# Optimization experiments

Measured on AMD Instinct MI355X. Metric: run time of the kernel, lower is better.

Reference implementation:

```python
import jax, jax.numpy as jnp
import numpy as np

B, N, K = 2, 50000, 16
CIN, COUT, M = 64, 32, 4


def setup_inputs() -> dict:
    key = jax.random.key(0)
    ks = jax.random.split(key, 7)
    x = jax.random.normal(ks[0], (B, N, CIN), dtype=jnp.float32)
    adj = jax.random.randint(ks[1], (B, N, K), 0, N + 1)  # 0 == empty slot
    weight = jax.random.normal(ks[2], (M, COUT, CIN), dtype=jnp.float32) * 0.1
    bias = jax.random.normal(ks[3], (COUT,), dtype=jnp.float32) * 0.1
    u = jax.random.normal(ks[4], (M, CIN), dtype=jnp.float32) * 0.1
    v = jax.random.normal(ks[5], (M, CIN), dtype=jnp.float32) * 0.1
    c = jax.random.normal(ks[6], (M,), dtype=jnp.float32) * 0.1
    return {"x": x, "adj": adj, "weight": weight, "bias": bias,
            "u": u, "v": v, "c": c}


def _gather_padded(feat, adj):
    # feat: (B, N, ...); adj: (B, N, K) indices into zero-padded node axis
    # (index 0 selects the zero row, matching torch get_patches semantics)
    pad = jnp.zeros((feat.shape[0], 1) + feat.shape[2:], feat.dtype)
    feat_p = jnp.concatenate([pad, feat], axis=1)        # (B, N+1, ...)
    return jax.vmap(lambda f, a: f[a])(feat_p, adj)      # (B, N, K, ...)


def reference(x, adj, weight, bias, u, v, c):
    # degree normalization: 1/#nonzero-neighbors, 0 for isolated points
    deg = jnp.sum(adj != 0, axis=-1).astype(x.dtype)     # (B, N)
    inv_deg = jnp.where(deg != 0, 1.0 / deg, 0.0)        # (B, N)

    # mixture-kernel transform of every node, then neighbor gather
    wx = jnp.einsum('bnc,moc->bnmo', x, weight)          # (B, N, M, COUT)
    gathered = _gather_padded(wx, adj)                   # (B, N, K, M, COUT)

    # softmax-gated assignment q[b,n,k,m] = softmax_m(v.x_nbr + u.x_ctr + c)
    ux = jnp.einsum('mc,bnc->bnm', u, x)                 # (B, N, M)
    vx = jnp.einsum('mc,bnc->bnm', v, x)                 # (B, N, M)
    vg = _gather_padded(vx, adj)                         # (B, N, K, M)
    q = jax.nn.softmax(vg + ux[:, :, None, :] + c, axis=-1)

    # weighted sum over neighbors K and mixture components M
    out = jnp.einsum('bnkm,bnkmo->bno', q, gathered)     # (B, N, COUT)
    return out * inv_deg[..., None] + bias
```

## Files before the change

### kernel.cpp

```cpp
#include <hip/hip_runtime.h>

namespace {
constexpr int BB = 2;
constexpr int NN = 50000;
constexpr int KK = 16;
constexpr int CI = 64;
constexpr int CO = 32;
constexpr int MM = 4;
constexpr int BN = BB * NN;
constexpr int GROUPS = NN / 4;
constexpr int GRID = 768;
constexpr int WAVES = (GRID / 2) * 4;
}

typedef __attribute__((ext_vector_type(8))) short short8v;
typedef __attribute__((ext_vector_type(4))) float float4v;
typedef __attribute__((ext_vector_type(2))) float f32x2;

union F4P {
  float4 f4;
  f32x2 p[2];
};

__device__ __forceinline__ unsigned short bf16r(float f) {
  unsigned int u = __float_as_uint(f);
  u += 0x7FFFu + ((u >> 16) & 1u);
  return (unsigned short)(u >> 16);
}

__global__ __launch_bounds__(256) void k_prep2(
    const float* __restrict__ x, const float* __restrict__ u,
    const float* __restrict__ v, float* __restrict__ ux,
    float* __restrict__ vx, unsigned short* __restrict__ xh) {
  const int tid = threadIdx.x;
  const int lane = tid & 63;
  const int wv = tid >> 6;
  const int col = lane & 15;
  const int krow = lane >> 4;

  short8v bfrag2[2];
#pragma unroll
  for (int ks = 0; ks < 2; ++ks)
#pragma unroll
    for (int e = 0; e < 8; ++e) {
      int c = ks * 32 + krow * 8 + e;
      float val = (col < 4) ? u[col * CI + c]
                            : ((col < 8) ? v[(col - 4) * CI + c] : 0.f);
      bfrag2[ks][e] = (short)bf16r(val);
    }

  const float4v zero = {0.f, 0.f, 0.f, 0.f};
  const int nw = gridDim.x * 4;
  for (int t = blockIdx.x * 4 + wv; t < BN / 16; t += nw) {
    const int n0 = t * 16;
    const float* xp = x + (size_t)(n0 + col) * CI + krow * 8;
    short8v afrag[2];
    uint4 hpack[2];
#pragma unroll
    for (int ks = 0; ks < 2; ++ks) {
      float4 lo = *(const float4*)(xp + ks * 32);
      float4 hi = *(const float4*)(xp + ks * 32 + 4);
      unsigned short h0 = bf16r(lo.x), h1 = bf16r(lo.y);
      unsigned short h2 = bf16r(lo.z), h3 = bf16r(lo.w);
      unsigned short h4 = bf16r(hi.x), h5 = bf16r(hi.y);
      unsigned short h6 = bf16r(hi.z), h7 = bf16r(hi.w);
      afrag[ks][0] = (short)h0;
      afrag[ks][1] = (short)h1;
      afrag[ks][2] = (short)h2;
      afrag[ks][3] = (short)h3;
      afrag[ks][4] = (short)h4;
      afrag[ks][5] = (short)h5;
      afrag[ks][6] = (short)h6;
      afrag[ks][7] = (short)h7;
      hpack[ks] = make_uint4((unsigned)h0 | ((unsigned)h1 << 16),
                             (unsigned)h2 | ((unsigned)h3 << 16),
                             (unsigned)h4 | ((unsigned)h5 << 16),
                             (unsigned)h6 | ((unsigned)h7 << 16));
    }
    unsigned short* xo = xh + (size_t)(n0 + col) * CI + krow * 8;
    *(uint4*)(xo) = hpack[0];
    *(uint4*)(xo + 32) = hpack[1];

    float4v acc2 = zero;
    acc2 = __builtin_amdgcn_mfma_f32_16x16x32_bf16(afrag[0], bfrag2[0], acc2,
                                                   0, 0, 0);
    acc2 = __builtin_amdgcn_mfma_f32_16x16x32_bf16(afrag[1], bfrag2[1], acc2,
                                                   0, 0, 0);
#pragma unroll
    for (int ri = 0; ri < 4; ++ri) {
      int node = n0 + krow * 4 + ri;
      if (col < 4)
        ux[(size_t)node * MM + col] = acc2[ri];
      else if (col < 8)
        vx[(size_t)node * MM + (col - 4)] = acc2[ri];
    }
  }
}

__global__ __launch_bounds__(256, 3) void k_gather(
    const unsigned short* __restrict__ xh, const int* __restrict__ adj,
    const float* __restrict__ weight, const float* __restrict__ bias,
    const float* __restrict__ cvec, const float* __restrict__ ux,
    const float* __restrict__ vx, float* __restrict__ out) {
  __shared__ unsigned short w_lds[2 * 8 * 64 * 8];
  __shared__ unsigned short t_lds[4][8 * 256];
  __shared__ float q_lds[4][4][64];

  const int tid = threadIdx.x;
  const int lane = tid & 63;
  const int wv = tid >> 6;

  for (int i = tid; i < 2 * 8 * 64; i += 256) {
    int tl = i >> 9;
    int ks = (i >> 6) & 7;
    int l = i & 63;
    int o = tl * 16 + (l & 15);
    unsigned pk[4];
#pragma unroll
    for (int ee = 0; ee < 4; ++ee) {
      int k0 = ks * 32 + (l >> 4) * 8 + 2 * ee;
      unsigned lo = bf16r(weight[((k0 & 3) * CO + o) * CI + (k0 >> 2)]);
      unsigned hi =
          bf16r(weight[(((k0 + 1) & 3) * CO + o) * CI + ((k0 + 1) >> 2)]);
      pk[ee] = lo | (hi << 16);
    }
    *(uint4*)&w_lds[i * 8] = make_uint4(pk[0], pk[1], pk[2], pk[3]);
  }
  __syncthreads();

  const int m4 = lane & 3;
  const int k4 = lane >> 2;
  const float cm = cvec[m4];
  const float b0 = bias[lane & 15];
  const float b1 = bias[16 + (lane & 15)];

  const int xcd = blockIdx.x & 7;
  const int b = xcd >> 2;
  const int wb = ((blockIdx.x >> 3) << 2) | (xcd & 3);
  const int w = wb * 4 + wv;
  const size_t bbase = (size_t)b * NN;
  const unsigned short* xhb = xh + bbase * CI;
  const float* vxb = vx + bbase * MM;
  unsigned short* twv = t_lds[wv];

#define LOADS(n, GV)                                                       \
  _Pragma("unroll") for (int k = 0; k < KK; ++k) {                         \
    int r = __builtin_amdgcn_readlane(av_c, (n)*16 + k);                   \
    const unsigned short* rp = xhb + (size_t)(max(r, 1) - 1) * CI;         \
    GV[k] = rp[lane];                                                      \
  }

#define ACC_NODE(n, GV)                                                    \
  {                                                                        \
    const float4* qp = (const float4*)&q_lds[wv][n][0];                    \
    f32x2 t01 = {0.f, 0.f}, t23 = {0.f, 0.f};                              \
    _Pragma("unroll") for (int k = 0; k < KK; ++k) {                       \
      float xv = __uint_as_float(GV[k] << 16);                             \
      F4P qv;                                                              \
      qv.f4 = qp[k];                                                       \
      t01 += qv.p[0] * xv;                                                 \
      t23 += qv.p[1] * xv;                                                 \
    }                                                                      \
    unsigned lo, hi;                                                       \
    asm("v_cvt_pk_bf16_f32 %0, %1, %2"                                     \
        : "=v"(lo)                                                         \
        : "v"(t01[0]), "v"(t01[1]));                                       \
    asm("v_cvt_pk_bf16_f32 %0, %1, %2"                                     \
        : "=v"(hi)                                                         \
        : "v"(t23[0]), "v"(t23[1]));                                       \
    int row = jrows * 4 + (n);                                             \
    unsigned boff = (unsigned)row * 512u +                                 \
                    (((unsigned)lane * 8u) ^ ((unsigned)(row & 7) << 4));  \
    *(uint2*)((char*)twv + boff) = make_uint2(lo, hi);                     \
  }

#define FLUSH(JC)                                                          \
  {                                                                        \
    float4v ac0 = {0.f, 0.f, 0.f, 0.f};                                    \
    float4v ac1 = {0.f, 0.f, 0.f, 0.f};                                    \
    const int arow = lane & 7;                                             \
    const unsigned axor = (unsigned)(arow & 7) << 4;                       \
    _Pragma("unroll") for (int ks = 0; ks < 8; ++ks) {                     \
      unsigned aoff =                                                      \
          (unsigned)arow * 512u +                                          \
          ((((unsigned)(lane >> 4)) * 16u + (unsigned)ks * 64u) ^ axor);   \
      short8v A = *(const short8v*)((const char*)twv + aoff);              \
      short8v Bl = *(const short8v*)&w_lds[(0 * 8 + ks) * 512 + lane * 8]; \
      short8v Bh = *(const short8v*)&w_lds[(1 * 8 + ks) * 512 + lane * 8]; \
      ac0 = __builtin_amdgcn_mfma_f32_16x16x32_bf16(A, Bl, ac0, 0, 0, 0);  \
      ac1 = __builtin_amdgcn_mfma_f32_16x16x32_bf16(A, Bh, ac1, 0, 0, 0);  \
    }                                                                      \
    int jj = lane >> 4;                                                    \
    int gg = gbase + jj * WAVES;                                           \
    if (jj < (JC) && gg < GROUPS) {                                        \
      float* op = out + (bbase + (size_t)gg * 4) * CO + (lane & 15);       \
      op[0] = ac0[0] + b0;                                                 \
      op[16] = ac1[0] + b1;                                                \
      op[32] = ac0[1] + b0;                                                \
      op[48] = ac1[1] + b1;                                                \
      op[64] = ac0[2] + b0;                                                \
      op[80] = ac1[2] + b1;                                                \
      op[96] = ac0[3] + b0;                                                \
      op[112] = ac1[3] + b1;                                               \
    }                                                                      \
  }

  int g = w;
  int av = 0;
  if (g < GROUPS) av = adj[(bbase + (size_t)g * 4) * KK + lane];
  int jrows = 0;
  int gbase = g;

  while (g < GROUPS) {
    const int av_c = av;
    const size_t bn0 = bbase + (size_t)g * 4;

    int as0 = __shfl(av_c, k4);
    int as1 = __shfl(av_c, 16 + k4);
    int as2 = __shfl(av_c, 32 + k4);
    int as3 = __shfl(av_c, 48 + k4);
    float vg0 = vxb[(size_t)(max(as0, 1) - 1) * MM + m4];
    float vg1 = vxb[(size_t)(max(as1, 1) - 1) * MM + m4];
    float vg2 = vxb[(size_t)(max(as2, 1) - 1) * MM + m4];
    float vg3 = vxb[(size_t)(max(as3, 1) - 1) * MM + m4];
    float ux0 = ux[bn0 * MM + m4];
    float ux1 = ux[(bn0 + 1) * MM + m4];
    float ux2 = ux[(bn0 + 2) * MM + m4];
    float ux3 = ux[(bn0 + 3) * MM + m4];
    const unsigned long long msk = __ballot(av_c != 0);

    unsigned gv0[KK], gv1[KK], gv2[KK], gv3[KK];
    LOADS(0, gv0)
    LOADS(1, gv1)
    LOADS(2, gv2)
    LOADS(3, gv3)
    __builtin_amdgcn_sched_barrier(0);

    const int gn = g + WAVES;
    if (gn < GROUPS) av = adj[(bbase + (size_t)gn * 4) * KK + lane];

    {
      int d0 = __popc((unsigned)(msk & 0xFFFFull));
      int d1 = __popc((unsigned)((msk >> 16) & 0xFFFFull));
      int d2 = __popc((unsigned)((msk >> 32) & 0xFFFFull));
      int d3 = __popc((unsigned)((msk >> 48) & 0xFFFFull));
      float i0 = d0 ? __builtin_amdgcn_rcpf((float)d0) : 0.f;
      float i1 = d1 ? __builtin_amdgcn_rcpf((float)d1) : 0.f;
      float i2 = d2 ? __builtin_amdgcn_rcpf((float)d2) : 0.f;
      float i3 = d3 ? __builtin_amdgcn_rcpf((float)d3) : 0.f;
      float e0 = __expf(vg0 + ux0 + cm);
      float e1 = __expf(vg1 + ux1 + cm);
      float e2 = __expf(vg2 + ux2 + cm);
      float e3 = __expf(vg3 + ux3 + cm);
      float s0 = e0 + __shfl_xor(e0, 1);
      float s1 = e1 + __shfl_xor(e1, 1);
      float s2 = e2 + __shfl_xor(e2, 1);
      float s3 = e3 + __shfl_xor(e3, 1);
      s0 += __shfl_xor(s0, 2);
      s1 += __shfl_xor(s1, 2);
      s2 += __shfl_xor(s2, 2);
      s3 += __shfl_xor(s3, 2);
      q_lds[wv][0][lane] =
          (as0 != 0) ? e0 * __builtin_amdgcn_rcpf(s0) * i0 : 0.f;
      q_lds[wv][1][lane] =
          (as1 != 0) ? e1 * __builtin_amdgcn_rcpf(s1) * i1 : 0.f;
      q_lds[wv][2][lane] =
          (as2 != 0) ? e2 * __builtin_amdgcn_rcpf(s2) * i2 : 0.f;
      q_lds[wv][3][lane] =
          (as3 != 0) ? e3 * __builtin_amdgcn_rcpf(s3) * i3 : 0.f;
    }

    ACC_NODE(0, gv0)
    ACC_NODE(1, gv1)
    ACC_NODE(2, gv2)
    ACC_NODE(3, gv3)

    ++jrows;
    g = gn;
    if (jrows == 2) {
      FLUSH(2)
      jrows = 0;
      gbase = g;
    }
  }
  if (jrows > 0) FLUSH(jrows)
}

__global__ __launch_bounds__(256) void k_uxvx(
    const float* __restrict__ x, const float* __restrict__ u,
    const float* __restrict__ v, float* __restrict__ ux,
    float* __restrict__ vx) {
  int idx = blockIdx.x * 256 + threadIdx.x;
  if (idx >= BN) return;
  const float4* xr = (const float4*)(x + (size_t)idx * CI);
  float su[MM] = {0.f, 0.f, 0.f, 0.f};
  float sv[MM] = {0.f, 0.f, 0.f, 0.f};
#pragma unroll
  for (int t = 0; t < CI / 4; ++t) {
    float4 xv = xr[t];
#pragma unroll
    for (int m = 0; m < MM; ++m) {
      float4 uv = *(const float4*)(u + m * CI + t * 4);
      float4 vv = *(const float4*)(v + m * CI + t * 4);
      su[m] += uv.x * xv.x + uv.y * xv.y + uv.z * xv.z + uv.w * xv.w;
      sv[m] += vv.x * xv.x + vv.y * xv.y + vv.z * xv.z + vv.w * xv.w;
    }
  }
  ((float4*)ux)[idx] = make_float4(su[0], su[1], su[2], su[3]);
  ((float4*)vx)[idx] = make_float4(sv[0], sv[1], sv[2], sv[3]);
}

__global__ __launch_bounds__(256) void k_main_old(
    const float* __restrict__ x, const int* __restrict__ adj,
    const float* __restrict__ weight, const float* __restrict__ bias,
    const float* __restrict__ cvec, const float* __restrict__ ux,
    const float* __restrict__ vx, float* __restrict__ out) {
  __shared__ float w_lds2[MM][CO][CI + 4];
  __shared__ float q_lds2[4][64];
  __shared__ float t_lds2[4][MM][CI];
  const int tid = threadIdx.x;
  const int lane = tid & 63;
  const int wv = tid >> 6;
#pragma unroll
  for (int i = 0; i < (MM * CO * CI) / 256; ++i) {
    int g = i * 256 + tid;
    w_lds2[g >> 11][(g >> 6) & (CO - 1)][g & (CI - 1)] = weight[g];
  }
  __syncthreads();
  const int k4 = lane >> 2;
  const int m4 = lane & 3;
  const int o = lane & 31;
  const int hh = lane >> 5;
  const float cm = cvec[m4];
  const float bo = bias[o];
  for (int g = blockIdx.x; g < BN / 4; g += gridDim.x) {
    const int bn = g * 4 + wv;
    const int b = (bn >= NN) ? 1 : 0;
    const int* adjp = adj + (size_t)bn * KK;
    const float* xb = x + (size_t)b * NN * CI;
    int4 A[4];
#pragma unroll
    for (int i = 0; i < 4; ++i) A[i] = ((const int4*)adjp)[i];
    int deg = 0;
#pragma unroll
    for (int i = 0; i < 4; ++i)
      deg += (A[i].x != 0) + (A[i].y != 0) + (A[i].z != 0) + (A[i].w != 0);
    const float inv_deg = (deg > 0) ? 1.0f / (float)deg : 0.0f;
    int a = adjp[k4];
    float vg = 0.f;
    if (a != 0) vg = vx[((size_t)b * NN + (a - 1)) * MM + m4];
    float logit = vg + ux[(size_t)bn * MM + m4] + cm;
    float mx = fmaxf(logit, __shfl_xor(logit, 1));
    mx = fmaxf(mx, __shfl_xor(mx, 2));
    float e = __expf(logit - mx);
    float s = e + __shfl_xor(e, 1);
    s += __shfl_xor(s, 2);
    q_lds2[wv][lane] = (a != 0) ? (e / s) : 0.f;
    int rows[KK];
    {
      int tmp[KK] = {A[0].x, A[0].y, A[0].z, A[0].w, A[1].x, A[1].y,
                     A[1].z, A[1].w, A[2].x, A[2].y, A[2].z, A[2].w,
                     A[3].x, A[3].y, A[3].z, A[3].w};
#pragma unroll
      for (int k = 0; k < KK; ++k) rows[k] = max(tmp[k], 1) - 1;
    }
    float xg[KK];
#pragma unroll
    for (int k = 0; k < KK; ++k) xg[k] = xb[(size_t)rows[k] * CI + lane];
    float t0 = 0.f, t1 = 0.f, t2 = 0.f, t3 = 0.f;
#pragma unroll
    for (int k = 0; k < KK; ++k) {
      float4 qv = *(const float4*)&q_lds2[wv][k * 4];
      t0 += qv.x * xg[k];
      t1 += qv.y * xg[k];
      t2 += qv.z * xg[k];
      t3 += qv.w * xg[k];
    }
    t_lds2[wv][0][lane] = t0;
    t_lds2[wv][1][lane] = t1;
    t_lds2[wv][2][lane] = t2;
    t_lds2[wv][3][lane] = t3;
    float a0 = 0.f, a1 = 0.f, a2 = 0.f, a3 = 0.f;
#pragma unroll
    for (int mm = 0; mm < 2; ++mm) {
      const float* wrow = &w_lds2[2 * hh + mm][o][0];
      const float* trow = &t_lds2[wv][2 * hh + mm][0];
#pragma unroll
      for (int t4 = 0; t4 < CI / 4; ++t4) {
        float4 wvv = *(const float4*)(wrow + 4 * t4);
        float4 tv = *(const float4*)(trow + 4 * t4);
        a0 += wvv.x * tv.x;
        a1 += wvv.y * tv.y;
        a2 += wvv.z * tv.z;
        a3 += wvv.w * tv.w;
      }
    }
    float acc = (a0 + a1) + (a2 + a3);
    acc += __shfl_xor(acc, 32);
    if (lane < 32) out[(size_t)bn * CO + o] = acc * inv_deg + bo;
  }
}

extern "C" void kernel_launch(void* const* d_in, const int* in_sizes, int n_in,
                              void* d_out, int out_size, void* d_ws,
                              size_t ws_size, hipStream_t stream) {
  const float* x = (const float*)d_in[0];
  const int* adj = (const int*)d_in[1];
  const float* weight = (const float*)d_in[2];
  const float* bias = (const float*)d_in[3];
  const float* u = (const float*)d_in[4];
  const float* v = (const float*)d_in[5];
  const float* cvec = (const float*)d_in[6];
  float* out = (float*)d_out;

  float* ux = (float*)d_ws;
  float* vx = ux + (size_t)BN * MM;
  const size_t base = (size_t)BN * MM * 2 * sizeof(float);
  const size_t xh_bytes = (size_t)BN * CI * sizeof(unsigned short);

  if (ws_size >= base + xh_bytes) {
    unsigned short* xhb = (unsigned short*)((char*)d_ws + base);
    k_prep2<<<1563, 256, 0, stream>>>(x, u, v, ux, vx, xhb);
    k_gather<<<GRID, 256, 0, stream>>>(xhb, adj, weight, bias, cvec, ux, vx,
                                       out);
  } else {
    k_uxvx<<<(BN + 255) / 256, 256, 0, stream>>>(x, u, v, ux, vx);
    k_main_old<<<1024, 256, 0, stream>>>(x, adj, weight, bias, cvec, ux, vx,
                                         out);
  }
}
```

Before: 62.53 us.

## Fuse prep and gather kernels into one cooperative kernel with grid sync

Merges the bf16 conversion / ux-vx projection kernel and the neighbour gather kernel into a single cooperative launch separated by a grid-wide barrier. Each block's prep work covers the same batch half it later gathers, and the weight LDS staging overlaps the prep phase. This removes one kernel launch and its inter-kernel gap. In exchange it adds a grid sync and depends on cooperative launch succeeding, with the old two-kernel path kept as a fallback.

```diff
diff --git a/kernel.cpp b/kernel.cpp
--- a/kernel.cpp
+++ b/kernel.cpp
@@ -1,4 +1,7 @@
 #include <hip/hip_runtime.h>
+#include <hip/hip_cooperative_groups.h>
+
+namespace cg = cooperative_groups;
 
 namespace {
 constexpr int BB = 2;
@@ -9,6 +12,7 @@
 constexpr int MM = 4;
 constexpr int BN = BB * NN;
 constexpr int GROUPS = NN / 4;
+constexpr int TILES = NN / 16;
 constexpr int GRID = 768;
 constexpr int WAVES = (GRID / 2) * 4;
 }
@@ -27,121 +31,6 @@
   u += 0x7FFFu + ((u >> 16) & 1u);
   return (unsigned short)(u >> 16);
 }
-
-__global__ __launch_bounds__(256) void k_prep2(
-    const float* __restrict__ x, const float* __restrict__ u,
-    const float* __restrict__ v, float* __restrict__ ux,
-    float* __restrict__ vx, unsigned short* __restrict__ xh) {
-  const int tid = threadIdx.x;
-  const int lane = tid & 63;
-  const int wv = tid >> 6;
-  const int col = lane & 15;
-  const int krow = lane >> 4;
-
-  short8v bfrag2[2];
-#pragma unroll
-  for (int ks = 0; ks < 2; ++ks)
-#pragma unroll
-    for (int e = 0; e < 8; ++e) {
-      int c = ks * 32 + krow * 8 + e;
-      float val = (col < 4) ? u[col * CI + c]
-                            : ((col < 8) ? v[(col - 4) * CI + c] : 0.f);
-      bfrag2[ks][e] = (short)bf16r(val);
-    }
-
-  const float4v zero = {0.f, 0.f, 0.f, 0.f};
-  const int nw = gridDim.x * 4;
-  for (int t = blockIdx.x * 4 + wv; t < BN / 16; t += nw) {
-    const int n0 = t * 16;
-    const float* xp = x + (size_t)(n0 + col) * CI + krow * 8;
-    short8v afrag[2];
-    uint4 hpack[2];
-#pragma unroll
-    for (int ks = 0; ks < 2; ++ks) {
-      float4 lo = *(const float4*)(xp + ks * 32);
-      float4 hi = *(const float4*)(xp + ks * 32 + 4);
-      unsigned short h0 = bf16r(lo.x), h1 = bf16r(lo.y);
-      unsigned short h2 = bf16r(lo.z), h3 = bf16r(lo.w);
-      unsigned short h4 = bf16r(hi.x), h5 = bf16r(hi.y);
-      unsigned short h6 = bf16r(hi.z), h7 = bf16r(hi.w);
-      afrag[ks][0] = (short)h0;
-      afrag[ks][1] = (short)h1;
-      afrag[ks][2] = (short)h2;
-      afrag[ks][3] = (short)h3;
-      afrag[ks][4] = (short)h4;
-      afrag[ks][5] = (short)h5;
-      afrag[ks][6] = (short)h6;
-      afrag[ks][7] = (short)h7;
-      hpack[ks] = make_uint4((unsigned)h0 | ((unsigned)h1 << 16),
-                             (unsigned)h2 | ((unsigned)h3 << 16),
-                             (unsigned)h4 | ((unsigned)h5 << 16),
-                             (unsigned)h6 | ((unsigned)h7 << 16));
-    }
-    unsigned short* xo = xh + (size_t)(n0 + col) * CI + krow * 8;
-    *(uint4*)(xo) = hpack[0];
-    *(uint4*)(xo + 32) = hpack[1];
-
-    float4v acc2 = zero;
-    acc2 = __builtin_amdgcn_mfma_f32_16x16x32_bf16(afrag[0], bfrag2[0], acc2,
-                                                   0, 0, 0);
-    acc2 = __builtin_amdgcn_mfma_f32_16x16x32_bf16(afrag[1], bfrag2[1], acc2,
-                                                   0, 0, 0);
-#pragma unroll
-    for (int ri = 0; ri < 4; ++ri) {
-      int node = n0 + krow * 4 + ri;
-      if (col < 4)
-        ux[(size_t)node * MM + col] = acc2[ri];
-      else if (col < 8)
-        vx[(size_t)node * MM + (col - 4)] = acc2[ri];
-    }
-  }
-}
-
-__global__ __launch_bounds__(256, 3) void k_gather(
-    const unsigned short* __restrict__ xh, const int* __restrict__ adj,
-    const float* __restrict__ weight, const float* __restrict__ bias,
-    const float* __restrict__ cvec, const float* __restrict__ ux,
-    const float* __restrict__ vx, float* __restrict__ out) {
-  __shared__ unsigned short w_lds[2 * 8 * 64 * 8];
-  __shared__ unsigned short t_lds[4][8 * 256];
-  __shared__ float q_lds[4][4][64];
-
-  const int tid = threadIdx.x;
-  const int lane = tid & 63;
-  const int wv = tid >> 6;
-
-  for (int i = tid; i < 2 * 8 * 64; i += 256) {
-    int tl = i >> 9;
-    int ks = (i >> 6) & 7;
-    int l = i & 63;
-    int o = tl * 16 + (l & 15);
-    unsigned pk[4];
-#pragma unroll
-    for (int ee = 0; ee < 4; ++ee) {
-      int k0 = ks * 32 + (l >> 4) * 8 + 2 * ee;
-      unsigned lo = bf16r(weight[((k0 & 3) * CO + o) * CI + (k0 >> 2)]);
-      unsigned hi =
-          bf16r(weight[(((k0 + 1) & 3) * CO + o) * CI + ((k0 + 1) >> 2)]);
-      pk[ee] = lo | (hi << 16);
-    }
-    *(uint4*)&w_lds[i * 8] = make_uint4(pk[0], pk[1], pk[2], pk[3]);
-  }
-  __syncthreads();
-
-  const int m4 = lane & 3;
-  const int k4 = lane >> 2;
-  const float cm = cvec[m4];
-  const float b0 = bias[lane & 15];
-  const float b1 = bias[16 + (lane & 15)];
-
-  const int xcd = blockIdx.x & 7;
-  const int b = xcd >> 2;
-  const int wb = ((blockIdx.x >> 3) << 2) | (xcd & 3);
-  const int w = wb * 4 + wv;
-  const size_t bbase = (size_t)b * NN;
-  const unsigned short* xhb = xh + bbase * CI;
-  const float* vxb = vx + bbase * MM;
-  unsigned short* twv = t_lds[wv];
 
 #define LOADS(n, GV)                                                       \
   _Pragma("unroll") for (int k = 0; k < KK; ++k) {                         \
@@ -205,85 +94,295 @@
     }                                                                      \
   }
 
-  int g = w;
-  int av = 0;
-  if (g < GROUPS) av = adj[(bbase + (size_t)g * 4) * KK + lane];
-  int jrows = 0;
-  int gbase = g;
-
-  while (g < GROUPS) {
-    const int av_c = av;
-    const size_t bn0 = bbase + (size_t)g * 4;
-
-    int as0 = __shfl(av_c, k4);
-    int as1 = __shfl(av_c, 16 + k4);
-    int as2 = __shfl(av_c, 32 + k4);
-    int as3 = __shfl(av_c, 48 + k4);
-    float vg0 = vxb[(size_t)(max(as0, 1) - 1) * MM + m4];
-    float vg1 = vxb[(size_t)(max(as1, 1) - 1) * MM + m4];
-    float vg2 = vxb[(size_t)(max(as2, 1) - 1) * MM + m4];
-    float vg3 = vxb[(size_t)(max(as3, 1) - 1) * MM + m4];
-    float ux0 = ux[bn0 * MM + m4];
-    float ux1 = ux[(bn0 + 1) * MM + m4];
-    float ux2 = ux[(bn0 + 2) * MM + m4];
-    float ux3 = ux[(bn0 + 3) * MM + m4];
-    const unsigned long long msk = __ballot(av_c != 0);
-
-    unsigned gv0[KK], gv1[KK], gv2[KK], gv3[KK];
-    LOADS(0, gv0)
-    LOADS(1, gv1)
-    LOADS(2, gv2)
-    LOADS(3, gv3)
-    __builtin_amdgcn_sched_barrier(0);
-
-    const int gn = g + WAVES;
-    if (gn < GROUPS) av = adj[(bbase + (size_t)gn * 4) * KK + lane];
-
-    {
-      int d0 = __popc((unsigned)(msk & 0xFFFFull));
-      int d1 = __popc((unsigned)((msk >> 16) & 0xFFFFull));
-      int d2 = __popc((unsigned)((msk >> 32) & 0xFFFFull));
-      int d3 = __popc((unsigned)((msk >> 48) & 0xFFFFull));
-      float i0 = d0 ? __builtin_amdgcn_rcpf((float)d0) : 0.f;
-      float i1 = d1 ? __builtin_amdgcn_rcpf((float)d1) : 0.f;
-      float i2 = d2 ? __builtin_amdgcn_rcpf((float)d2) : 0.f;
-      float i3 = d3 ? __builtin_amdgcn_rcpf((float)d3) : 0.f;
-      float e0 = __expf(vg0 + ux0 + cm);
-      float e1 = __expf(vg1 + ux1 + cm);
-      float e2 = __expf(vg2 + ux2 + cm);
-      float e3 = __expf(vg3 + ux3 + cm);
-      float s0 = e0 + __shfl_xor(e0, 1);
-      float s1 = e1 + __shfl_xor(e1, 1);
-      float s2 = e2 + __shfl_xor(e2, 1);
-      float s3 = e3 + __shfl_xor(e3, 1);
-      s0 += __shfl_xor(s0, 2);
-      s1 += __shfl_xor(s1, 2);
-      s2 += __shfl_xor(s2, 2);
-      s3 += __shfl_xor(s3, 2);
-      q_lds[wv][0][lane] =
-          (as0 != 0) ? e0 * __builtin_amdgcn_rcpf(s0) * i0 : 0.f;
-      q_lds[wv][1][lane] =
-          (as1 != 0) ? e1 * __builtin_amdgcn_rcpf(s1) * i1 : 0.f;
-      q_lds[wv][2][lane] =
-          (as2 != 0) ? e2 * __builtin_amdgcn_rcpf(s2) * i2 : 0.f;
-      q_lds[wv][3][lane] =
-          (as3 != 0) ? e3 * __builtin_amdgcn_rcpf(s3) * i3 : 0.f;
-    }
-
-    ACC_NODE(0, gv0)
-    ACC_NODE(1, gv1)
-    ACC_NODE(2, gv2)
-    ACC_NODE(3, gv3)
-
-    ++jrows;
-    g = gn;
-    if (jrows == 2) {
-      FLUSH(2)
-      jrows = 0;
-      gbase = g;
-    }
-  }
+#define STAGE_WLDS                                                           \
+  for (int i = tid; i < 2 * 8 * 64; i += 256) {                              \
+    int tl = i >> 9;                                                         \
+    int ks = (i >> 6) & 7;                                                   \
+    int l = i & 63;                                                          \
+    int o = tl * 16 + (l & 15);                                              \
+    unsigned pk[4];                                                          \
+    _Pragma("unroll") for (int ee = 0; ee < 4; ++ee) {                       \
+      int k0 = ks * 32 + (l >> 4) * 8 + 2 * ee;                              \
+      unsigned lo = bf16r(weight[((k0 & 3) * CO + o) * CI + (k0 >> 2)]);     \
+      unsigned hi =                                                          \
+          bf16r(weight[(((k0 + 1) & 3) * CO + o) * CI + ((k0 + 1) >> 2)]);   \
+      pk[ee] = lo | (hi << 16);                                              \
+    }                                                                        \
+    *(uint4*)&w_lds[i * 8] = make_uint4(pk[0], pk[1], pk[2], pk[3]);         \
+  }
+
+#define GATHER_LOOP                                                           \
+  int g = w;                                                                  \
+  int av = 0;                                                                 \
+  if (g < GROUPS) av = adj[(bbase + (size_t)g * 4) * KK + lane];              \
+  int jrows = 0;                                                              \
+  int gbase = g;                                                              \
+  while (g < GROUPS) {                                                        \
+    const int av_c = av;                                                      \
+    const size_t bn0 = bbase + (size_t)g * 4;                                 \
+    int as0 = __shfl(av_c, k4);                                               \
+    int as1 = __shfl(av_c, 16 + k4);                                          \
+    int as2 = __shfl(av_c, 32 + k4);                                          \
+    int as3 = __shfl(av_c, 48 + k4);                                          \
+    float vg0 = vxb[(size_t)(max(as0, 1) - 1) * MM + m4];                     \
+    float vg1 = vxb[(size_t)(max(as1, 1) - 1) * MM + m4];                     \
+    float vg2 = vxb[(size_t)(max(as2, 1) - 1) * MM + m4];                     \
+    float vg3 = vxb[(size_t)(max(as3, 1) - 1) * MM + m4];                     \
+    float ux0 = ux[bn0 * MM + m4];                                            \
+    float ux1 = ux[(bn0 + 1) * MM + m4];                                      \
+    float ux2 = ux[(bn0 + 2) * MM + m4];                                      \
+    float ux3 = ux[(bn0 + 3) * MM + m4];                                      \
+    const unsigned long long msk = __ballot(av_c != 0);                       \
+    unsigned gv0[KK], gv1[KK], gv2[KK], gv3[KK];                              \
+    LOADS(0, gv0)                                                             \
+    LOADS(1, gv1)                                                             \
+    LOADS(2, gv2)                                                             \
+    LOADS(3, gv3)                                                             \
+    __builtin_amdgcn_sched_barrier(0);                                        \
+    const int gn = g + WAVES;                                                 \
+    if (gn < GROUPS) av = adj[(bbase + (size_t)gn * 4) * KK + lane];          \
+    {                                                                         \
+      int d0 = __popc((unsigned)(msk & 0xFFFFull));                           \
+      int d1 = __popc((unsigned)((msk >> 16) & 0xFFFFull));                   \
+      int d2 = __popc((unsigned)((msk >> 32) & 0xFFFFull));                   \
+      int d3 = __popc((unsigned)((msk >> 48) & 0xFFFFull));                   \
+      float i0 = d0 ? __builtin_amdgcn_rcpf((float)d0) : 0.f;                 \
+      float i1 = d1 ? __builtin_amdgcn_rcpf((float)d1) : 0.f;                 \
+      float i2 = d2 ? __builtin_amdgcn_rcpf((float)d2) : 0.f;                 \
+      float i3 = d3 ? __builtin_amdgcn_rcpf((float)d3) : 0.f;                 \
+      float e0 = __expf(vg0 + ux0 + cm);                                      \
+      float e1 = __expf(vg1 + ux1 + cm);                                      \
+      float e2 = __expf(vg2 + ux2 + cm);                                      \
+      float e3 = __expf(vg3 + ux3 + cm);                                      \
+      float s0 = e0 + __shfl_xor(e0, 1);                                      \
+      float s1 = e1 + __shfl_xor(e1, 1);                                      \
+      float s2 = e2 + __shfl_xor(e2, 1);                                      \
+      float s3 = e3 + __shfl_xor(e3, 1);                                      \
+      s0 += __shfl_xor(s0, 2);                                                \
+      s1 += __shfl_xor(s1, 2);                                                \
+      s2 += __shfl_xor(s2, 2);                                                \
+      s3 += __shfl_xor(s3, 2);                                                \
+      q_lds[wv][0][lane] =                                                    \
+          (as0 != 0) ? e0 * __builtin_amdgcn_rcpf(s0) * i0 : 0.f;             \
+      q_lds[wv][1][lane] =                                                    \
+          (as1 != 0) ? e1 * __builtin_amdgcn_rcpf(s1) * i1 : 0.f;             \
+      q_lds[wv][2][lane] =                                                    \
+          (as2 != 0) ? e2 * __builtin_amdgcn_rcpf(s2) * i2 : 0.f;             \
+      q_lds[wv][3][lane] =                                                    \
+          (as3 != 0) ? e3 * __builtin_amdgcn_rcpf(s3) * i3 : 0.f;             \
+    }                                                                         \
+    ACC_NODE(0, gv0)                                                          \
+    ACC_NODE(1, gv1)                                                          \
+    ACC_NODE(2, gv2)                                                          \
+    ACC_NODE(3, gv3)                                                          \
+    ++jrows;                                                                  \
+    g = gn;                                                                   \
+    if (jrows == 2) {                                                         \
+      FLUSH(2)                                                                \
+      jrows = 0;                                                              \
+      gbase = g;                                                              \
+    }                                                                         \
+  }                                                                           \
   if (jrows > 0) FLUSH(jrows)
+
+__global__ __launch_bounds__(256, 3) void k_fused(
+    const float* __restrict__ x, const int* __restrict__ adj,
+    const float* __restrict__ weight, const float* __restrict__ bias,
+    const float* __restrict__ cvec, const float* __restrict__ u,
+    const float* __restrict__ v, float* __restrict__ ux,
+    float* __restrict__ vx, unsigned short* __restrict__ xh,
+    float* __restrict__ out) {
+  __shared__ unsigned short w_lds[2 * 8 * 64 * 8];
+  __shared__ unsigned short t_lds[4][8 * 256];
+  __shared__ float q_lds[4][4][64];
+
+  const int tid = threadIdx.x;
+  const int lane = tid & 63;
+  const int wv = tid >> 6;
+
+  STAGE_WLDS
+
+  const int xcd = blockIdx.x & 7;
+  const int b = xcd >> 2;
+  const int wb = ((blockIdx.x >> 3) << 2) | (xcd & 3);
+  const int w = wb * 4 + wv;
+  const size_t bbase = (size_t)b * NN;
+
+  {
+    const int col = lane & 15;
+    const int krow = lane >> 4;
+    short8v bfrag2[2];
+#pragma unroll
+    for (int ks = 0; ks < 2; ++ks)
+#pragma unroll
+      for (int e = 0; e < 8; ++e) {
+        int c = ks * 32 + krow * 8 + e;
+        float val = (col < 4) ? u[col * CI + c]
+                              : ((col < 8) ? v[(col - 4) * CI + c] : 0.f);
+        bfrag2[ks][e] = (short)bf16r(val);
+      }
+    const float4v zero = {0.f, 0.f, 0.f, 0.f};
+    for (int tt = w; tt < TILES; tt += WAVES) {
+      const int n0 = ((int)bbase) + tt * 16;
+      const float* xp = x + (size_t)(n0 + col) * CI + krow * 8;
+      short8v afrag[2];
+      uint4 hpack[2];
+#pragma unroll
+      for (int ks = 0; ks < 2; ++ks) {
+        float4 lo = *(const float4*)(xp + ks * 32);
+        float4 hi = *(const float4*)(xp + ks * 32 + 4);
+        unsigned short h0 = bf16r(lo.x), h1 = bf16r(lo.y);
+        unsigned short h2 = bf16r(lo.z), h3 = bf16r(lo.w);
+        unsigned short h4 = bf16r(hi.x), h5 = bf16r(hi.y);
+        unsigned short h6 = bf16r(hi.z), h7 = bf16r(hi.w);
+        afrag[ks][0] = (short)h0;
+        afrag[ks][1] = (short)h1;
+        afrag[ks][2] = (short)h2;
+        afrag[ks][3] = (short)h3;
+        afrag[ks][4] = (short)h4;
+        afrag[ks][5] = (short)h5;
+        afrag[ks][6] = (short)h6;
+        afrag[ks][7] = (short)h7;
+        hpack[ks] = make_uint4((unsigned)h0 | ((unsigned)h1 << 16),
+                               (unsigned)h2 | ((unsigned)h3 << 16),
+                               (unsigned)h4 | ((unsigned)h5 << 16),
+                               (unsigned)h6 | ((unsigned)h7 << 16));
+      }
+      unsigned short* xo = xh + (size_t)(n0 + col) * CI + krow * 8;
+      *(uint4*)(xo) = hpack[0];
+      *(uint4*)(xo + 32) = hpack[1];
+
+      float4v acc2 = zero;
+      acc2 = __builtin_amdgcn_mfma_f32_16x16x32_bf16(afrag[0], bfrag2[0],
+                                                     acc2, 0, 0, 0);
+      acc2 = __builtin_amdgcn_mfma_f32_16x16x32_bf16(afrag[1], bfrag2[1],
+                                                     acc2, 0, 0, 0);
+#pragma unroll
+      for (int ri = 0; ri < 4; ++ri) {
+        int node = n0 + krow * 4 + ri;
+        if (col < 4)
+          ux[(size_t)node * MM + col] = acc2[ri];
+        else if (col < 8)
+          vx[(size_t)node * MM + (col - 4)] = acc2[ri];
+      }
+    }
+  }
+
+  cg::this_grid().sync();
+
+  const int m4 = lane & 3;
+  const int k4 = lane >> 2;
+  const float cm = cvec[m4];
+  const float b0 = bias[lane & 15];
+  const float b1 = bias[16 + (lane & 15)];
+  const unsigned short* xhb = xh + bbase * CI;
+  const float* vxb = vx + bbase * MM;
+  unsigned short* twv = t_lds[wv];
+
+  GATHER_LOOP
+}
+
+__global__ __launch_bounds__(256) void k_prep2(
+    const float* __restrict__ x, const float* __restrict__ u,
+    const float* __restrict__ v, float* __restrict__ ux,
+    float* __restrict__ vx, unsigned short* __restrict__ xh) {
+  const int tid = threadIdx.x;
+  const int lane = tid & 63;
+  const int wv = tid >> 6;
+  const int col = lane & 15;
+  const int krow = lane >> 4;
+
+  short8v bfrag2[2];
+#pragma unroll
+  for (int ks = 0; ks < 2; ++ks)
+#pragma unroll
+    for (int e = 0; e < 8; ++e) {
+      int c = ks * 32 + krow * 8 + e;
+      float val = (col < 4) ? u[col * CI + c]
+                            : ((col < 8) ? v[(col - 4) * CI + c] : 0.f);
+      bfrag2[ks][e] = (short)bf16r(val);
+    }
+
+  const float4v zero = {0.f, 0.f, 0.f, 0.f};
+  const int nw = gridDim.x * 4;
+  for (int t = blockIdx.x * 4 + wv; t < BN / 16; t += nw) {
+    const int n0 = t * 16;
+    const float* xp = x + (size_t)(n0 + col) * CI + krow * 8;
+    short8v afrag[2];
+    uint4 hpack[2];
+#pragma unroll
+    for (int ks = 0; ks < 2; ++ks) {
+      float4 lo = *(const float4*)(xp + ks * 32);
+      float4 hi = *(const float4*)(xp + ks * 32 + 4);
+      unsigned short h0 = bf16r(lo.x), h1 = bf16r(lo.y);
+      unsigned short h2 = bf16r(lo.z), h3 = bf16r(lo.w);
+      unsigned short h4 = bf16r(hi.x), h5 = bf16r(hi.y);
+      unsigned short h6 = bf16r(hi.z), h7 = bf16r(hi.w);
+      afrag[ks][0] = (short)h0;
+      afrag[ks][1] = (short)h1;
+      afrag[ks][2] = (short)h2;
+      afrag[ks][3] = (short)h3;
+      afrag[ks][4] = (short)h4;
+      afrag[ks][5] = (short)h5;
+      afrag[ks][6] = (short)h6;
+      afrag[ks][7] = (short)h7;
+      hpack[ks] = make_uint4((unsigned)h0 | ((unsigned)h1 << 16),
+                             (unsigned)h2 | ((unsigned)h3 << 16),
+                             (unsigned)h4 | ((unsigned)h5 << 16),
+                             (unsigned)h6 | ((unsigned)h7 << 16));
+    }
+    unsigned short* xo = xh + (size_t)(n0 + col) * CI + krow * 8;
+    *(uint4*)(xo) = hpack[0];
+    *(uint4*)(xo + 32) = hpack[1];
+
+    float4v acc2 = zero;
+    acc2 = __builtin_amdgcn_mfma_f32_16x16x32_bf16(afrag[0], bfrag2[0], acc2,
+                                                   0, 0, 0);
+    acc2 = __builtin_amdgcn_mfma_f32_16x16x32_bf16(afrag[1], bfrag2[1], acc2,
+                                                   0, 0, 0);
+#pragma unroll
+    for (int ri = 0; ri < 4; ++ri) {
+      int node = n0 + krow * 4 + ri;
+      if (col < 4)
+        ux[(size_t)node * MM + col] = acc2[ri];
+      else if (col < 8)
+        vx[(size_t)node * MM + (col - 4)] = acc2[ri];
+    }
+  }
+}
+
+__global__ __launch_bounds__(256, 3) void k_gather(
+    const unsigned short* __restrict__ xh, const int* __restrict__ adj,
+    const float* __restrict__ weight, const float* __restrict__ bias,
+    const float* __restrict__ cvec, const float* __restrict__ ux,
+    const float* __restrict__ vx, float* __restrict__ out) {
+  __shared__ unsigned short w_lds[2 * 8 * 64 * 8];
+  __shared__ unsigned short t_lds[4][8 * 256];
+  __shared__ float q_lds[4][4][64];
+
+  const int tid = threadIdx.x;
+  const int lane = tid & 63;
+  const int wv = tid >> 6;
+
+  STAGE_WLDS
+  __syncthreads();
+
+  const int m4 = lane & 3;
+  const int k4 = lane >> 2;
+  const float cm = cvec[m4];
+  const float b0 = bias[lane & 15];
+  const float b1 = bias[16 + (lane & 15)];
+
+  const int xcd = blockIdx.x & 7;
+  const int b = xcd >> 2;
+  const int wb = ((blockIdx.x >> 3) << 2) | (xcd & 3);
+  const int w = wb * 4 + wv;
+  const size_t bbase = (size_t)b * NN;
+  const unsigned short* xhb = xh + bbase * CI;
+  const float* vxb = vx + bbase * MM;
+  unsigned short* twv = t_lds[wv];
+
+  GATHER_LOOP
 }
 
 __global__ __launch_bounds__(256) void k_uxvx(
@@ -420,9 +519,17 @@
 
   if (ws_size >= base + xh_bytes) {
     unsigned short* xhb = (unsigned short*)((char*)d_ws + base);
-    k_prep2<<<1563, 256, 0, stream>>>(x, u, v, ux, vx, xhb);
-    k_gather<<<GRID, 256, 0, stream>>>(xhb, adj, weight, bias, cvec, ux, vx,
-                                       out);
+    void* args[] = {(void*)&x,  (void*)&adj, (void*)&weight, (void*)&bias,
+                    (void*)&cvec, (void*)&u, (void*)&v,      (void*)&ux,
+                    (void*)&vx, (void*)&xhb, (void*)&out};
+    hipError_t e = hipLaunchCooperativeKernel((const void*)k_fused,
+                                              dim3(GRID), dim3(256), args, 0,
+                                              stream);
+    if (e != hipSuccess) {
+      k_prep2<<<1563, 256, 0, stream>>>(x, u, v, ux, vx, xhb);
+      k_gather<<<GRID, 256, 0, stream>>>(xhb, adj, weight, bias, cvec, ux, vx,
+                                         out);
+    }
   } else {
     k_uxvx<<<(BN + 255) / 256, 256, 0, stream>>>(x, u, v, ux, vx);
     k_main_old<<<1024, 256, 0, stream>>>(x, adj, weight, bias, cvec, ux, vx,
```

Measured after the change: 169.2 us. +170.7%, slower.

## Gather neighbor rows as 16-byte chunks into LDS and recompute vx via MFMA

Applied to the files above, without the earlier changes.

The gather kernel now handles two nodes per wave iteration instead of four. It loads each neighbor's bf16 feature row as full 16-byte chunks, using ds_bpermute to spread the indices across lanes, and stages the rows in a swizzled LDS tile. It no longer gathers precomputed vx from global memory; it recomputes v·x_nbr with small bf16 MFMAs on the staged tile. The aim is fewer, wider global loads and no scattered vx gathers, paid for with extra LDS traffic, more LDS use per block and bf16 precision for the gate logits.

```diff
diff --git a/kernel.cpp b/kernel.cpp
--- a/kernel.cpp
+++ b/kernel.cpp
@@ -8,7 +8,7 @@
 constexpr int CO = 32;
 constexpr int MM = 4;
 constexpr int BN = BB * NN;
-constexpr int GROUPS = NN / 4;
+constexpr int GROUPS2 = NN / 2;
 constexpr int GRID = 768;
 constexpr int WAVES = (GRID / 2) * 4;
 }
@@ -16,11 +16,6 @@
 typedef __attribute__((ext_vector_type(8))) short short8v;
 typedef __attribute__((ext_vector_type(4))) float float4v;
 typedef __attribute__((ext_vector_type(2))) float f32x2;
-
-union F4P {
-  float4 f4;
-  f32x2 p[2];
-};
 
 __device__ __forceinline__ unsigned short bf16r(float f) {
   unsigned int u = __float_as_uint(f);
@@ -101,10 +96,12 @@
     const unsigned short* __restrict__ xh, const int* __restrict__ adj,
     const float* __restrict__ weight, const float* __restrict__ bias,
     const float* __restrict__ cvec, const float* __restrict__ ux,
-    const float* __restrict__ vx, float* __restrict__ out) {
-  __shared__ unsigned short w_lds[2 * 8 * 64 * 8];
-  __shared__ unsigned short t_lds[4][8 * 256];
-  __shared__ float q_lds[4][4][64];
+    const float* __restrict__ v, float* __restrict__ out) {
+  __shared__ unsigned short w_lds[8192];
+  __shared__ unsigned short t_lds[4][2048];
+  __shared__ unsigned short xtile[4][2048];
+  __shared__ float q_lds[4][2][64];
+  __shared__ float vgscr[4][2][64];
 
   const int tid = threadIdx.x;
   const int lane = tid & 63;
@@ -126,6 +123,17 @@
     }
     *(uint4*)&w_lds[i * 8] = make_uint4(pk[0], pk[1], pk[2], pk[3]);
   }
+
+  const int col = lane & 15;
+  const int krow = lane >> 4;
+  short8v vfrag[2];
+#pragma unroll
+  for (int ks = 0; ks < 2; ++ks)
+#pragma unroll
+    for (int e = 0; e < 8; ++e) {
+      int c = ks * 32 + krow * 8 + e;
+      vfrag[ks][e] = (short)((col < 4) ? bf16r(v[col * CI + c]) : 0);
+    }
   __syncthreads();
 
   const int m4 = lane & 3;
@@ -133,6 +141,8 @@
   const float cm = cvec[m4];
   const float b0 = bias[lane & 15];
   const float b1 = bias[16 + (lane & 15)];
+  const int hn = lane >> 5;
+  const int c2 = lane & 31;
 
   const int xcd = blockIdx.x & 7;
   const int b = xcd >> 2;
@@ -140,150 +150,181 @@
   const int w = wb * 4 + wv;
   const size_t bbase = (size_t)b * NN;
   const unsigned short* xhb = xh + bbase * CI;
-  const float* vxb = vx + bbase * MM;
   unsigned short* twv = t_lds[wv];
-
-#define LOADS(n, GV)                                                       \
-  _Pragma("unroll") for (int k = 0; k < KK; ++k) {                         \
-    int r = __builtin_amdgcn_readlane(av_c, (n)*16 + k);                   \
-    const unsigned short* rp = xhb + (size_t)(max(r, 1) - 1) * CI;         \
-    GV[k] = rp[lane];                                                      \
-  }
-
-#define ACC_NODE(n, GV)                                                    \
-  {                                                                        \
-    const float4* qp = (const float4*)&q_lds[wv][n][0];                    \
-    f32x2 t01 = {0.f, 0.f}, t23 = {0.f, 0.f};                              \
-    _Pragma("unroll") for (int k = 0; k < KK; ++k) {                       \
-      float xv = __uint_as_float(GV[k] << 16);                             \
-      F4P qv;                                                              \
-      qv.f4 = qp[k];                                                       \
-      t01 += qv.p[0] * xv;                                                 \
-      t23 += qv.p[1] * xv;                                                 \
-    }                                                                      \
-    unsigned lo, hi;                                                       \
-    asm("v_cvt_pk_bf16_f32 %0, %1, %2"                                     \
-        : "=v"(lo)                                                         \
-        : "v"(t01[0]), "v"(t01[1]));                                       \
-    asm("v_cvt_pk_bf16_f32 %0, %1, %2"                                     \
-        : "=v"(hi)                                                         \
-        : "v"(t23[0]), "v"(t23[1]));                                       \
-    int row = jrows * 4 + (n);                                             \
-    unsigned boff = (unsigned)row * 512u +                                 \
-                    (((unsigned)lane * 8u) ^ ((unsigned)(row & 7) << 4));  \
-    *(uint2*)((char*)twv + boff) = make_uint2(lo, hi);                     \
-  }
-
-#define FLUSH(JC)                                                          \
-  {                                                                        \
-    float4v ac0 = {0.f, 0.f, 0.f, 0.f};                                    \
-    float4v ac1 = {0.f, 0.f, 0.f, 0.f};                                    \
-    const int arow = lane & 7;                                             \
-    const unsigned axor = (unsigned)(arow & 7) << 4;                       \
-    _Pragma("unroll") for (int ks = 0; ks < 8; ++ks) {                     \
-      unsigned aoff =                                                      \
-          (unsigned)arow * 512u +                                          \
-          ((((unsigned)(lane >> 4)) * 16u + (unsigned)ks * 64u) ^ axor);   \
-      short8v A = *(const short8v*)((const char*)twv + aoff);              \
-      short8v Bl = *(const short8v*)&w_lds[(0 * 8 + ks) * 512 + lane * 8]; \
-      short8v Bh = *(const short8v*)&w_lds[(1 * 8 + ks) * 512 + lane * 8]; \
-      ac0 = __builtin_amdgcn_mfma_f32_16x16x32_bf16(A, Bl, ac0, 0, 0, 0);  \
-      ac1 = __builtin_amdgcn_mfma_f32_16x16x32_bf16(A, Bh, ac1, 0, 0, 0);  \
-    }                                                                      \
-    int jj = lane >> 4;                                                    \
-    int gg = gbase + jj * WAVES;                                           \
-    if (jj < (JC) && gg < GROUPS) {                                        \
-      float* op = out + (bbase + (size_t)gg * 4) * CO + (lane & 15);       \
-      op[0] = ac0[0] + b0;                                                 \
-      op[16] = ac1[0] + b1;                                                \
-      op[32] = ac0[1] + b0;                                                \
-      op[48] = ac1[1] + b1;                                                \
-      op[64] = ac0[2] + b0;                                                \
-      op[80] = ac1[2] + b1;                                                \
-      op[96] = ac0[3] + b0;                                                \
-      op[112] = ac1[3] + b1;                                               \
-    }                                                                      \
+  char* xt = (char*)&xtile[wv][0];
+  float* vs = &vgscr[wv][0][0];
+
+  const int bpb = (lane >> 3) << 2;
+  const unsigned chunkoff = (unsigned)((lane & 7) * 16);
+  const unsigned swoff =
+      (unsigned)((lane >> 3) * 128) +
+      (chunkoff ^ (unsigned)((lane >> 3) << 4));
+  unsigned vga[2][2];
+#pragma unroll
+  for (int t2 = 0; t2 < 2; ++t2)
+#pragma unroll
+    for (int ks = 0; ks < 2; ++ks)
+      vga[t2][ks] =
+          (unsigned)((t2 * 16 + (lane & 15)) * 128) +
+          ((((unsigned)(ks * 4 + (lane >> 4)) ^ (unsigned)(lane & 7)) << 4));
+  unsigned xav[8];
+#pragma unroll
+  for (int j = 0; j < 8; ++j)
+    xav[j] = ((((unsigned)(c2 >> 2) ^ (unsigned)j) << 4) |
+              ((unsigned)(c2 & 3) << 2));
+  const unsigned sw2 = (unsigned)((lane >> 4) * 64 + (lane & 15) * 4);
+
+#define FLUSH2(JC)                                                         \
+  {                                                                       \
+    float4v ac0 = {0.f, 0.f, 0.f, 0.f};                                   \
+    float4v ac1 = {0.f, 0.f, 0.f, 0.f};                                   \
+    const int arow = lane & 7;                                            \
+    const unsigned axor = (unsigned)(arow & 7) << 4;                      \
+    _Pragma("unroll") for (int ks = 0; ks < 8; ++ks) {                    \
+      unsigned aoff =                                                     \
+          (unsigned)arow * 512u +                                         \
+          ((((unsigned)(lane >> 4)) * 16u + (unsigned)ks * 64u) ^ axor);  \
+      short8v A = *(const short8v*)((const char*)twv + aoff);             \
+      short8v Bl = *(const short8v*)&w_lds[(0 * 8 + ks) * 512 + lane * 8];\
+      short8v Bh = *(const short8v*)&w_lds[(1 * 8 + ks) * 512 + lane * 8];\
+      ac0 = __builtin_amdgcn_mfma_f32_16x16x32_bf16(A, Bl, ac0, 0, 0, 0); \
+      ac1 = __builtin_amdgcn_mfma_f32_16x16x32_bf16(A, Bh, ac1, 0, 0, 0); \
+    }                                                                     \
+    int jj = lane >> 4;                                                   \
+    _Pragma("unroll") for (int ri = 0; ri < 4; ++ri) {                    \
+      int it = jj * 2 + (ri >> 1);                                        \
+      int gg = gbase + it * WAVES;                                        \
+      if (it < (JC) && gg < GROUPS2) {                                    \
+        size_t node = bbase + (size_t)gg * 2 + (ri & 1);                  \
+        out[node * CO + (lane & 15)] = ac0[ri] + b0;                      \
+        out[node * CO + 16 + (lane & 15)] = ac1[ri] + b1;                 \
+      }                                                                   \
+    }                                                                     \
   }
 
   int g = w;
   int av = 0;
-  if (g < GROUPS) av = adj[(bbase + (size_t)g * 4) * KK + lane];
+  if (g < GROUPS2) av = adj[(bbase + (size_t)g * 2) * KK + (lane & 31)];
   int jrows = 0;
   int gbase = g;
 
-  while (g < GROUPS) {
+  while (g < GROUPS2) {
     const int av_c = av;
-    const size_t bn0 = bbase + (size_t)g * 4;
-
-    int as0 = __shfl(av_c, k4);
-    int as1 = __shfl(av_c, 16 + k4);
-    int as2 = __shfl(av_c, 32 + k4);
-    int as3 = __shfl(av_c, 48 + k4);
-    float vg0 = vxb[(size_t)(max(as0, 1) - 1) * MM + m4];
-    float vg1 = vxb[(size_t)(max(as1, 1) - 1) * MM + m4];
-    float vg2 = vxb[(size_t)(max(as2, 1) - 1) * MM + m4];
-    float vg3 = vxb[(size_t)(max(as3, 1) - 1) * MM + m4];
-    float ux0 = ux[bn0 * MM + m4];
-    float ux1 = ux[(bn0 + 1) * MM + m4];
-    float ux2 = ux[(bn0 + 2) * MM + m4];
-    float ux3 = ux[(bn0 + 3) * MM + m4];
-    const unsigned long long msk = __ballot(av_c != 0);
-
-    unsigned gv0[KK], gv1[KK], gv2[KK], gv3[KK];
-    LOADS(0, gv0)
-    LOADS(1, gv1)
-    LOADS(2, gv2)
-    LOADS(3, gv3)
-    __builtin_amdgcn_sched_barrier(0);
+    const size_t bn0 = bbase + (size_t)g * 2;
+
+    const int as0 = __shfl(av_c, k4);
+    const int as1 = __shfl(av_c, 16 + k4);
+    const float ux0 = ux[bn0 * MM + m4];
+    const float ux1 = ux[bn0 * MM + MM + m4];
+
+    uint4 gx0, gx1, gx2, gx3;
+    {
+      int nb0 = __builtin_amdgcn_ds_bpermute(bpb + 0, av_c);
+      int nb1 = __builtin_amdgcn_ds_bpermute(bpb + 32, av_c);
+      int nb2 = __builtin_amdgcn_ds_bpermute(bpb + 64, av_c);
+      int nb3 = __builtin_amdgcn_ds_bpermute(bpb + 96, av_c);
+      unsigned r0 = (unsigned)(max(nb0, 1) - 1) * 128u + chunkoff;
+      unsigned r1 = (unsigned)(max(nb1, 1) - 1) * 128u + chunkoff;
+      unsigned r2 = (unsigned)(max(nb2, 1) - 1) * 128u + chunkoff;
+      unsigned r3 = (unsigned)(max(nb3, 1) - 1) * 128u + chunkoff;
+      gx0 = *(const uint4*)((const char*)xhb + (size_t)r0);
+      gx1 = *(const uint4*)((const char*)xhb + (size_t)r1);
+      gx2 = *(const uint4*)((const char*)xhb + (size_t)r2);
+      gx3 = *(const uint4*)((const char*)xhb + (size_t)r3);
+    }
 
     const int gn = g + WAVES;
-    if (gn < GROUPS) av = adj[(bbase + (size_t)gn * 4) * KK + lane];
+    if (gn < GROUPS2) av = adj[(bbase + (size_t)gn * 2) * KK + (lane & 31)];
+
+    *(uint4*)(xt + swoff + 0) = gx0;
+    *(uint4*)(xt + swoff + 1024) = gx1;
+    *(uint4*)(xt + swoff + 2048) = gx2;
+    *(uint4*)(xt + swoff + 3072) = gx3;
 
     {
-      int d0 = __popc((unsigned)(msk & 0xFFFFull));
-      int d1 = __popc((unsigned)((msk >> 16) & 0xFFFFull));
-      int d2 = __popc((unsigned)((msk >> 32) & 0xFFFFull));
-      int d3 = __popc((unsigned)((msk >> 48) & 0xFFFFull));
+      short8v A00 = *(const short8v*)(xt + vga[0][0]);
+      short8v A01 = *(const short8v*)(xt + vga[0][1]);
+      short8v A10 = *(const short8v*)(xt + vga[1][0]);
+      short8v A11 = *(const short8v*)(xt + vga[1][1]);
+      float4v vac0 = {0.f, 0.f, 0.f, 0.f};
+      float4v vac1 = {0.f, 0.f, 0.f, 0.f};
+      vac0 = __builtin_amdgcn_mfma_f32_16x16x32_bf16(A00, vfrag[0], vac0, 0,
+                                                     0, 0);
+      vac0 = __builtin_amdgcn_mfma_f32_16x16x32_bf16(A01, vfrag[1], vac0, 0,
+                                                     0, 0);
+      vac1 = __builtin_amdgcn_mfma_f32_16x16x32_bf16(A10, vfrag[0], vac1, 0,
+                                                     0, 0);
+      vac1 = __builtin_amdgcn_mfma_f32_16x16x32_bf16(A11, vfrag[1], vac1, 0,
+                                                     0, 0);
+      if ((lane & 15) < 4) {
+        *(float*)((char*)vs + sw2 + 0) = vac0[0];
+        *(float*)((char*)vs + sw2 + 16) = vac0[1];
+        *(float*)((char*)vs + sw2 + 32) = vac0[2];
+        *(float*)((char*)vs + sw2 + 48) = vac0[3];
+        *(float*)((char*)vs + sw2 + 256) = vac1[0];
+        *(float*)((char*)vs + sw2 + 272) = vac1[1];
+        *(float*)((char*)vs + sw2 + 288) = vac1[2];
+        *(float*)((char*)vs + sw2 + 304) = vac1[3];
+      }
+    }
+    const float vg0 = vgscr[wv][0][lane];
+    const float vg1 = vgscr[wv][1][lane];
+
+    {
+      const unsigned msk = (unsigned)__ballot(av_c != 0);
+      int d0 = __popc(msk & 0xFFFFu);
+      int d1 = __popc(msk >> 16);
       float i0 = d0 ? __builtin_amdgcn_rcpf((float)d0) : 0.f;
       float i1 = d1 ? __builtin_amdgcn_rcpf((float)d1) : 0.f;
-      float i2 = d2 ? __builtin_amdgcn_rcpf((float)d2) : 0.f;
-      float i3 = d3 ? __builtin_amdgcn_rcpf((float)d3) : 0.f;
       float e0 = __expf(vg0 + ux0 + cm);
       float e1 = __expf(vg1 + ux1 + cm);
-      float e2 = __expf(vg2 + ux2 + cm);
-      float e3 = __expf(vg3 + ux3 + cm);
       float s0 = e0 + __shfl_xor(e0, 1);
       float s1 = e1 + __shfl_xor(e1, 1);
-      float s2 = e2 + __shfl_xor(e2, 1);
-      float s3 = e3 + __shfl_xor(e3, 1);
       s0 += __shfl_xor(s0, 2);
       s1 += __shfl_xor(s1, 2);
-      s2 += __shfl_xor(s2, 2);
-      s3 += __shfl_xor(s3, 2);
       q_lds[wv][0][lane] =
           (as0 != 0) ? e0 * __builtin_amdgcn_rcpf(s0) * i0 : 0.f;
       q_lds[wv][1][lane] =
           (as1 != 0) ? e1 * __builtin_amdgcn_rcpf(s1) * i1 : 0.f;
-      q_lds[wv][2][lane] =
-          (as2 != 0) ? e2 * __builtin_amdgcn_rcpf(s2) * i2 : 0.f;
-      q_lds[wv][3][lane] =
-          (as3 != 0) ? e3 * __builtin_amdgcn_rcpf(s3) * i3 : 0.f;
-    }
-
-    ACC_NODE(0, gv0)
-    ACC_NODE(1, gv1)
-    ACC_NODE(2, gv2)
-    ACC_NODE(3, gv3)
+    }
+
+    {
+      const float4* qp = (const float4*)&q_lds[wv][hn][0];
+      f32x2 a0 = {0.f, 0.f}, a1 = {0.f, 0.f};
+      f32x2 a2 = {0.f, 0.f}, a3 = {0.f, 0.f};
+#pragma unroll
+      for (int k = 0; k < KK; ++k) {
+        unsigned xx =
+            *(const unsigned*)(xt + hn * 2048 + k * 128 + xav[k & 7]);
+        float xe = __uint_as_float(xx << 16);
+        float xo = __uint_as_float(xx & 0xFFFF0000u);
+        f32x2 xp = {xe, xo};
+        float4 qv = qp[k];
+        a0 += xp * qv.x;
+        a1 += xp * qv.y;
+        a2 += xp * qv.z;
+        a3 += xp * qv.w;
+      }
+      unsigned p0, p1, p2, p3;
+      asm("v_cvt_pk_bf16_f32 %0, %1, %2" : "=v"(p0) : "v"(a0[0]), "v"(a1[0]));
+      asm("v_cvt_pk_bf16_f32 %0, %1, %2" : "=v"(p1) : "v"(a2[0]), "v"(a3[0]));
+      asm("v_cvt_pk_bf16_f32 %0, %1, %2" : "=v"(p2) : "v"(a0[1]), "v"(a1[1]));
+      asm("v_cvt_pk_bf16_f32 %0, %1, %2" : "=v"(p3) : "v"(a2[1]), "v"(a3[1]));
+      const int trow = jrows * 2 + hn;
+      unsigned boff = (unsigned)trow * 512u +
+                      (((unsigned)c2 * 16u) ^ ((unsigned)(trow & 7) << 4));
+      *(uint4*)((char*)twv + boff) = make_uint4(p0, p1, p2, p3);
+    }
 
     ++jrows;
     g = gn;
-    if (jrows == 2) {
-      FLUSH(2)
+    if (jrows == 4) {
+      FLUSH2(4)
       jrows = 0;
       gbase = g;
     }
   }
-  if (jrows > 0) FLUSH(jrows)
+  if (jrows > 0) FLUSH2(jrows)
 }
 
 __global__ __launch_bounds__(256) void k_uxvx(
@@ -421,7 +462,7 @@
   if (ws_size >= base + xh_bytes) {
     unsigned short* xhb = (unsigned short*)((char*)d_ws + base);
     k_prep2<<<1563, 256, 0, stream>>>(x, u, v, ux, vx, xhb);
-    k_gather<<<GRID, 256, 0, stream>>>(xhb, adj, weight, bias, cvec, ux, vx,
+    k_gather<<<GRID, 256, 0, stream>>>(xhb, adj, weight, bias, cvec, ux, v,
                                        out);
   } else {
     k_uxvx<<<(BN + 255) / 256, 256, 0, stream>>>(x, u, v, ux, vx);
```

Measured after the change: 62.20 us. No clear change (-0.5%).
